# Kernel tuning notes

Hardware: AMD Instinct MI355X
Metric: run time of the kernel (lower is better)

## Reference

```python
import jax, jax.numpy as jnp
import numpy as np

IMG = 800.0
STRIDE = 16
P = 7            # pool_out_size
SAMP = 2         # RoIAlign samples per bin per dim (sampling_ratio=-1 approximated as 2)
SCALE = 1.0 / 16.0   # feature_compress
TOPN = 6000      # score_top_n
NMS_TOPN = 300   # nms_top_n
NMS_TH = 0.7
NC = 21


def _anchors(H, W):
    ratios = np.array([0.5, 1.0, 2.0])
    scales = np.array([8.0, 16.0, 32.0])
    ws = (STRIDE * scales[None, :] / np.sqrt(ratios)[:, None]).reshape(-1)  # [9]
    hs = (STRIDE * scales[None, :] * np.sqrt(ratios)[:, None]).reshape(-1)
    cx = (np.arange(W) + 0.5) * STRIDE
    cy = (np.arange(H) + 0.5) * STRIDE
    cxg, cyg = np.meshgrid(cx, cy)  # [H,W]
    a = np.stack([cxg[..., None] - ws / 2, cyg[..., None] - hs / 2,
                  cxg[..., None] + ws / 2, cyg[..., None] + hs / 2], axis=-1)  # [H,W,9,4]
    return jnp.asarray(a.reshape(-1, 4), jnp.float32)


def _decode(anchors, deltas):
    aw = anchors[:, 2] - anchors[:, 0]
    ah = anchors[:, 3] - anchors[:, 1]
    ax = anchors[:, 0] + aw / 2
    ay = anchors[:, 1] + ah / 2
    cx = ax + deltas[:, 0] * aw
    cy = ay + deltas[:, 1] * ah
    w = aw * jnp.exp(deltas[:, 2])
    h = ah * jnp.exp(deltas[:, 3])
    boxes = jnp.stack([cx - w / 2, cy - h / 2, cx + w / 2, cy + h / 2], axis=1)
    return jnp.clip(boxes, 0.0, IMG)


def _iou(b):
    area = (b[:, 2] - b[:, 0]) * (b[:, 3] - b[:, 1])
    lt = jnp.maximum(b[:, None, :2], b[None, :, :2])
    rb = jnp.minimum(b[:, None, 2:], b[None, :, 2:])
    wh = jnp.clip(rb - lt, 0.0)
    inter = wh[..., 0] * wh[..., 1]
    return inter / (area[:, None] + area[None, :] - inter + 1e-9)


def _nms_select(boxes, scores):
    # boxes already sorted descending by scores; greedy NMS, fixed-size output indices
    iou = _iou(boxes)
    n = boxes.shape[0]
    rng = jnp.arange(n)

    def body(i, sup):
        keep_i = jnp.logical_not(sup[i])
        return sup | (keep_i & (iou[i] > NMS_TH) & (rng > i))

    sup = jax.lax.fori_loop(0, n, body, jnp.zeros((n,), bool))
    sel = jnp.where(sup, -jnp.inf, scores)
    _, idx = jax.lax.top_k(sel, NMS_TOPN)
    return idx


def _roi_align(feat, rois):
    # feat [C,H,W], rois [R,4] in image coords
    C, H, W = feat.shape
    off = (jnp.arange(P * SAMP, dtype=jnp.float32) + 0.5) / SAMP  # bin-unit positions

    def one(box):
        x1, y1, x2, y2 = box * SCALE
        xs = x1 + off * (x2 - x1) / P  # [P*SAMP]
        ys = y1 + off * (y2 - y1) / P
        x0 = jnp.floor(xs)
        y0 = jnp.floor(ys)
        lx = xs - x0
        ly = ys - y0
        x0i = jnp.clip(x0, 0, W - 1).astype(jnp.int32)
        x1i = jnp.clip(x0 + 1, 0, W - 1).astype(jnp.int32)
        y0i = jnp.clip(y0, 0, H - 1).astype(jnp.int32)
        y1i = jnp.clip(y0 + 1, 0, H - 1).astype(jnp.int32)

        def g(yi, xi):
            return feat[:, yi[:, None], xi[None, :]]  # [C,PS,PS]

        v = (g(y0i, x0i) * ((1 - ly)[:, None] * (1 - lx)[None, :])[None]
             + g(y0i, x1i) * ((1 - ly)[:, None] * lx[None, :])[None]
             + g(y1i, x0i) * (ly[:, None] * (1 - lx)[None, :])[None]
             + g(y1i, x1i) * (ly[:, None] * lx[None, :])[None])
        return v.reshape(C, P, SAMP, P, SAMP).mean(axis=(2, 4))  # [C,P,P]

    return jax.vmap(one)(rois)  # [R,C,P,P]


def reference(image, w_feat, b_feat, w_rpn, b_rpn, w_score, b_score,
              w_delta, b_delta, w_fc7, b_fc7, w_cls, b_cls, w_reg, b_reg):
    # backbone: stride-16 patchifying conv -> [1,512,50,50]
    feat = jax.lax.conv_general_dilated(image, w_feat, (STRIDE, STRIDE), 'VALID') \
           + b_feat[None, :, None, None]
    H, W = feat.shape[2], feat.shape[3]
    anchors = _anchors(H, W)  # [H*W*9, 4]

    # RPN: 3x3 conv + relu, 1x1 score/delta heads
    h = jax.nn.relu(jax.lax.conv_general_dilated(feat, w_rpn, (1, 1), 'SAME')
                    + b_rpn[None, :, None, None])
    sc = jnp.einsum('bchw,oc->bhwo', h, w_score) + b_score  # [1,H,W,9*2]
    dl = jnp.einsum('bchw,oc->bhwo', h, w_delta) + b_delta  # [1,H,W,9*4]
    rpn_score = jax.nn.softmax(sc.reshape(-1, 2), axis=-1)  # [HW*9, 2]
    rpn_delta = dl.reshape(-1, 4)

    # compute_proposals: decode, clip, top-k by fg score, greedy NMS
    fg = rpn_score[:, 1]
    boxes = _decode(anchors, rpn_delta)
    top_s, top_i = jax.lax.top_k(jax.lax.stop_gradient(fg), TOPN)
    cand = boxes[top_i]
    keep = _nms_select(jax.lax.stop_gradient(cand), top_s)
    rois = cand[keep]  # [300,4]

    # RoIAlign + heads
    pool = _roi_align(feat[0], rois)  # [300,512,7,7]
    fc7 = jax.nn.relu(pool.reshape(pool.shape[0], -1) @ w_fc7.T + b_fc7)  # [300,4096]
    score = fc7 @ w_cls.T + b_cls  # [300,21]
    bbox = (fc7 @ w_reg.T + b_reg).reshape(-1, NC, 4)  # [300,21,4]
    return score, bbox


def setup_inputs():
    key = jax.random.key(0)
    ks = jax.random.split(key, 9)

    def rn(k, shape, s=0.02):
        return jax.random.normal(k, shape, jnp.float32) * s

    z = lambda n: jnp.zeros((n,), jnp.float32)
    return {
        'image': jax.random.normal(ks[0], (1, 3, 800, 800), jnp.float32),
        'w_feat': rn(ks[1], (512, 3, 16, 16)), 'b_feat': z(512),
        'w_rpn': rn(ks[2], (512, 512, 3, 3)), 'b_rpn': z(512),
        'w_score': rn(ks[3], (18, 512)), 'b_score': z(18),
        'w_delta': rn(ks[4], (36, 512), 0.01), 'b_delta': z(36),
        'w_fc7': rn(ks[5], (4096, 512 * 7 * 7), 0.01), 'b_fc7': z(4096),
        'w_cls': rn(ks[6], (21, 4096)), 'b_cls': z(21),
        'w_reg': rn(ks[7], (84, 4096)), 'b_reg': z(84),
    }
```

## Files before the change

kernel.cpp:

```cpp
#include <hip/hip_runtime.h>
#include <cstdint>

typedef short  short8  __attribute__((ext_vector_type(8)));
typedef unsigned short ushort8 __attribute__((ext_vector_type(8)));
typedef _Float16 half8 __attribute__((ext_vector_type(8)));
typedef float  f32x4   __attribute__((ext_vector_type(4)));
typedef unsigned long long u64;

#define NPOS 2500
#define NA   22500
#define TOPN 6000
#define NKEEP 300
#define NBUCK 65536
#define THRESH 512
#define NSUB 8192
#define KSTEPS 392
#define RANKBLKS 22

__device__ __forceinline__ unsigned short f2bf(float f) {
  unsigned u = __float_as_uint(f);
  return (unsigned short)((u + 0x7FFFu + ((u >> 16) & 1u)) >> 16);
}

__global__ __launch_bounds__(256) void k1_gemm(const float* __restrict__ Asrc,
    const float* __restrict__ Bsrc, float* __restrict__ P, int klen,
    const float* __restrict__ wr, unsigned short* __restrict__ Whi,
    unsigned short* __restrict__ Wlo, int* __restrict__ histbuf)
{
  {
    int gtid = ((blockIdx.z * gridDim.y + blockIdx.y) * gridDim.x + blockIdx.x) * 256
             + threadIdx.x;
    int nth = gridDim.x * gridDim.y * gridDim.z * 256;
    if (gtid < NBUCK + 1 + 256) histbuf[gtid] = 0;
    for (int e = gtid; e < 512 * 4608; e += nth) {
      int n = e / 4608, r = e - n * 4608;
      int s = r >> 9, c = r & 511;
      float w = wr[n * 4608 + c * 9 + s] * 1024.f;
      _Float16 hi = (_Float16)w;
      _Float16 lo = (_Float16)(w - (float)hi);
      ((_Float16*)Whi)[e] = hi;
      ((_Float16*)Wlo)[e] = lo;
    }
  }

  __shared__ float As[32][128];
  __shared__ float Bs[32][132];
  int tid = threadIdx.x;
  int tx = tid & 15, ty = tid >> 4;
  int mt = blockIdx.x, nt = blockIdx.y;
  int m0 = mt * 128, n0 = nt * 128;
  int kbase = blockIdx.z * klen;

  int m_loc = tid & 127;
  int half = tid >> 7;
  int gm = m0 + m_loc;
  int y = gm / 50, x = gm - y * 50;
  bool mok = gm < NPOS;

  float acc[8][8] = {};

  for (int kt = 0; kt < klen; kt += 32) {
    int kb = kbase + kt;
    int k0 = kb + half * 16;
    int ci = k0 >> 8, r = (k0 >> 4) & 15;
    const float* src = Asrc + ci * 640000 + (y * 16 + r) * 800 + x * 16;
#pragma unroll
    for (int j = 0; j < 4; ++j) {
      float4 v = mok ? *(const float4*)(src + j * 4) : make_float4(0.f, 0.f, 0.f, 0.f);
      As[half * 16 + j * 4 + 0][m_loc] = v.x;
      As[half * 16 + j * 4 + 1][m_loc] = v.y;
      As[half * 16 + j * 4 + 2][m_loc] = v.z;
      As[half * 16 + j * 4 + 3][m_loc] = v.w;
    }
#pragma unroll
    for (int i = 0; i < 4; ++i) {
      int e = i * 256 + tid;
      int k4 = e & 7, n = e >> 3;
      float4 v = *(const float4*)(Bsrc + (size_t)(n0 + n) * 768 + kb + k4 * 4);
      Bs[k4 * 4 + 0][n] = v.x;
      Bs[k4 * 4 + 1][n] = v.y;
      Bs[k4 * 4 + 2][n] = v.z;
      Bs[k4 * 4 + 3][n] = v.w;
    }
    __syncthreads();
#pragma unroll 8
    for (int k = 0; k < 32; ++k) {
      float4 a0 = *(const float4*)&As[k][ty * 8];
      float4 a1 = *(const float4*)&As[k][ty * 8 + 4];
      float4 b0 = *(const float4*)&Bs[k][tx * 8];
      float4 b1 = *(const float4*)&Bs[k][tx * 8 + 4];
      float av[8] = {a0.x, a0.y, a0.z, a0.w, a1.x, a1.y, a1.z, a1.w};
      float bv[8] = {b0.x, b0.y, b0.z, b0.w, b1.x, b1.y, b1.z, b1.w};
#pragma unroll
      for (int i2 = 0; i2 < 8; ++i2)
#pragma unroll
        for (int j2 = 0; j2 < 8; ++j2) acc[i2][j2] += av[i2] * bv[j2];
    }
    __syncthreads();
  }
  float* Pp = P + ((size_t)(blockIdx.z * 20 + mt) * 4 + nt) * 16384;
#pragma unroll
  for (int i = 0; i < 8; ++i) {
    float4 v0 = {acc[i][0], acc[i][1], acc[i][2], acc[i][3]};
    float4 v1 = {acc[i][4], acc[i][5], acc[i][6], acc[i][7]};
    *(float4*)&Pp[(ty * 8 + i) * 128 + tx * 8] = v0;
    *(float4*)&Pp[(ty * 8 + i) * 128 + tx * 8 + 4] = v1;
  }
}

__global__ __launch_bounds__(256) void kred1(const float* __restrict__ P,
    const float* __restrict__ bias, float* __restrict__ feat_t,
    unsigned short* __restrict__ Fhi, unsigned short* __restrict__ Flo, int KS)
{
  int idx = blockIdx.x * 256 + threadIdx.x;
  if (idx >= NPOS * 512) return;
  int m = idx >> 9, n = idx & 511;
  int mt = m >> 7, ml = m & 127, nt = n >> 7, nl = n & 127;
  float s = 0.f;
  for (int z = 0; z < KS; ++z)
    s += P[(((size_t)(z * 20 + mt) * 4 + nt) << 14) + ml * 128 + nl];
  s += bias[n];
  feat_t[idx] = s;
  float fs = s * 2048.f;
  _Float16 hi = (_Float16)fs;
  _Float16 lo = (_Float16)(fs - (float)hi);
  ((_Float16*)Fhi)[idx] = hi;
  ((_Float16*)Flo)[idx] = lo;
}

__global__ __launch_bounds__(256) void k2_mfma(
    const unsigned short* __restrict__ Fhi, const unsigned short* __restrict__ Flo,
    const unsigned short* __restrict__ Whi, const unsigned short* __restrict__ Wlo,
    float* __restrict__ partial)
{
  __shared__ __align__(16) unsigned short As[8 * 162 * 8];
  __shared__ __align__(16) unsigned short Bs[8 * 130 * 8];
  int tid = threadIdx.x;
  int lane = tid & 63, wn = tid >> 6;
  int nt = blockIdx.x, mt = blockIdx.y, z = blockIdx.z;
  int n0 = nt * 128;

  f32x4 acc[10][2];
#pragma unroll
  for (int i = 0; i < 10; ++i)
#pragma unroll
    for (int j = 0; j < 2; ++j) acc[i][j] = (f32x4){0.f, 0.f, 0.f, 0.f};

  int yv[5], xv[5], slotA[5], gof[5];
  bool okv[5];
#pragma unroll
  for (int j = 0; j < 5; ++j) {
    int o = j * 256 + tid;
    int m = o >> 3, g = o & 7;
    int gm = mt * 160 + m;
    okv[j] = gm < NPOS;
    yv[j] = gm / 50;
    xv[j] = gm - yv[j] * 50;
    slotA[j] = g * 162 + m;
    gof[j] = g * 8;
  }

  ushort8 aR[5], bR[4];

  auto LOAD = [&](int t) {
    int tg = z * 27 + t;
    const unsigned short* Asrc = (tg < 144) ? Fhi : Flo;
    const unsigned short* Bsrc = (tg < 72 || tg >= 144) ? Whi : Wlo;
    int ks = (tg >= 144) ? (tg - 144) : ((tg >= 72) ? (tg - 72) : tg);
    int ki = ks * 64;
    int srow = ki >> 9;
    int c0 = ki & 511;
    int dy = srow / 3, dx = srow - (srow / 3) * 3;
#pragma unroll
    for (int j = 0; j < 5; ++j) {
      int yy = yv[j] + dy - 1, xx = xv[j] + dx - 1;
      ushort8 v = {0, 0, 0, 0, 0, 0, 0, 0};
      if (okv[j] && (unsigned)yy < 50u && (unsigned)xx < 50u)
        v = *(const ushort8*)(Asrc + (size_t)(yy * 50 + xx) * 512 + c0 + gof[j]);
      aR[j] = v;
    }
#pragma unroll
    for (int j = 0; j < 4; ++j) {
      int o = j * 256 + tid;
      int n = o >> 3, g = o & 7;
      bR[j] = *(const ushort8*)(Bsrc + (size_t)(n0 + n) * 4608 + ki + g * 8);
    }
  };

  LOAD(0);
  for (int t = 0; t < 27; ++t) {
    __syncthreads();
#pragma unroll
    for (int j = 0; j < 5; ++j)
      ((ushort8*)As)[slotA[j]] = aR[j];
#pragma unroll
    for (int j = 0; j < 4; ++j) {
      int o = j * 256 + tid;
      ((ushort8*)Bs)[(o & 7) * 130 + (o >> 3)] = bR[j];
    }
    __syncthreads();
    if (t + 1 < 27) LOAD(t + 1);
#pragma unroll
    for (int kk = 0; kk < 2; ++kk) {
      int g = kk * 4 + (lane >> 4);
      half8 b0 = ((const half8*)Bs)[g * 130 + wn * 32 + (lane & 15)];
      half8 b1 = ((const half8*)Bs)[g * 130 + wn * 32 + 16 + (lane & 15)];
#pragma unroll
      for (int fm = 0; fm < 10; ++fm) {
        half8 a = ((const half8*)As)[g * 162 + fm * 16 + (lane & 15)];
        acc[fm][0] = __builtin_amdgcn_mfma_f32_16x16x32_f16(a, b0, acc[fm][0], 0, 0, 0);
        acc[fm][1] = __builtin_amdgcn_mfma_f32_16x16x32_f16(a, b1, acc[fm][1], 0, 0, 0);
      }
    }
  }
  float* P = partial + ((size_t)(z * 16 + mt) * 4 + nt) * 20480;
#pragma unroll
  for (int fm = 0; fm < 10; ++fm)
#pragma unroll
    for (int fn = 0; fn < 2; ++fn)
#pragma unroll
      for (int r = 0; r < 4; ++r) {
        int m = fm * 16 + (lane >> 4) * 4 + r;
        int n = wn * 32 + fn * 16 + (lane & 15);
        P[m * 128 + n] = acc[fm][fn][r];
      }
}

__global__ __launch_bounds__(256) void k3_fused(const float* __restrict__ P,
    const float* __restrict__ b_rpn,
    const float* __restrict__ w_score, const float* __restrict__ b_score,
    const float* __restrict__ w_delta, const float* __restrict__ b_delta,
    float4* __restrict__ boxes, u64* __restrict__ keys, int* __restrict__ hist)
{
  __shared__ float4 hv4[4][128];
  __shared__ float outv[4][54];
  int grp = threadIdx.x >> 6, lane = threadIdx.x & 63;
  int p = blockIdx.x * 4 + grp;
  int mt = p / 160, ml = p - mt * 160;
  int nt = lane >> 4;
  int nl8 = (lane * 8) & 127;

  float4 a0 = make_float4(0.f, 0.f, 0.f, 0.f);
  float4 a1 = make_float4(0.f, 0.f, 0.f, 0.f);
  for (int z = 0; z < 8; ++z) {
    const float* Pb = P + ((size_t)(z * 16 + mt) * 4 + nt) * 20480 + ml * 128 + nl8;
    float4 v0 = *(const float4*)Pb;
    float4 v1 = *(const float4*)(Pb + 4);
    a0.x += v0.x; a0.y += v0.y; a0.z += v0.z; a0.w += v0.w;
    a1.x += v1.x; a1.y += v1.y; a1.z += v1.z; a1.w += v1.w;
  }
  const float SC = 1.f / 2097152.f;
  const float4 b0 = *(const float4*)(b_rpn + lane * 8);
  const float4 b1 = *(const float4*)(b_rpn + lane * 8 + 4);
  float4 h0 = make_float4(fmaxf(a0.x * SC + b0.x, 0.f), fmaxf(a0.y * SC + b0.y, 0.f),
                          fmaxf(a0.z * SC + b0.z, 0.f), fmaxf(a0.w * SC + b0.w, 0.f));
  float4 h1 = make_float4(fmaxf(a1.x * SC + b1.x, 0.f), fmaxf(a1.y * SC + b1.y, 0.f),
                          fmaxf(a1.z * SC + b1.z, 0.f), fmaxf(a1.w * SC + b1.w, 0.f));
  hv4[grp][lane * 2] = h0;
  hv4[grp][lane * 2 + 1] = h1;
  __syncthreads();

  if (lane < 54) {
    const float* w; float bb;
    if (lane < 18) { w = w_score + lane * 512; bb = b_score[lane]; }
    else           { w = w_delta + (lane - 18) * 512; bb = b_delta[lane - 18]; }
    const float4* w4 = (const float4*)w;
    float s = 0.f;
#pragma unroll 4
    for (int q = 0; q < 128; ++q) {
      float4 a = hv4[grp][q], b = w4[q];
      s += a.x * b.x + a.y * b.y + a.z * b.z + a.w * b.w;
    }
    outv[grp][lane] = s + bb;
  }
  __syncthreads();
  if (lane < 9) {
    int k = lane;
    float s0 = outv[grp][2 * k], s1 = outv[grp][2 * k + 1];
    float mx = fmaxf(s0, s1);
    float e0 = expf(s0 - mx), e1 = expf(s1 - mx);
    float f = e1 / (e0 + e1);
    double ratio = (k < 3) ? 0.5 : ((k < 6) ? 1.0 : 2.0);
    int si = k - (k / 3) * 3;
    double scale = (si == 0) ? 8.0 : ((si == 1) ? 16.0 : 32.0);
    double sq = sqrt(ratio);
    double wsd = 16.0 * scale / sq;
    double hsd = 16.0 * scale * sq;
    int y = p / 50, x = p - (p / 50) * 50;
    double cxd = ((double)x + 0.5) * 16.0;
    double cyd = ((double)y + 0.5) * 16.0;
    float ax1 = (float)(cxd - wsd / 2.0);
    float ay1 = (float)(cyd - hsd / 2.0);
    float ax2 = (float)(cxd + wsd / 2.0);
    float ay2 = (float)(cyd + hsd / 2.0);
    float aw = ax2 - ax1, ah = ay2 - ay1;
    float axc = ax1 + aw * 0.5f, ayc = ay1 + ah * 0.5f;
    float d0 = outv[grp][18 + 4 * k], d1 = outv[grp][18 + 4 * k + 1];
    float d2 = outv[grp][18 + 4 * k + 2], d3 = outv[grp][18 + 4 * k + 3];
    float cx = axc + d0 * aw, cy = ayc + d1 * ah;
    float bw = aw * expf(d2), bh = ah * expf(d3);
    float bx1 = fminf(fmaxf(cx - bw * 0.5f, 0.f), 800.f);
    float by1 = fminf(fmaxf(cy - bh * 0.5f, 0.f), 800.f);
    float bx2 = fminf(fmaxf(cx + bw * 0.5f, 0.f), 800.f);
    float by2 = fminf(fmaxf(cy + bh * 0.5f, 0.f), 800.f);
    int idx = p * 9 + k;
    boxes[idx] = make_float4(bx1, by1, bx2, by2);
    u64 key = ((u64)__float_as_uint(f) << 32) | (u64)(0xFFFFFFFFu - (unsigned)idx);
    keys[idx] = key;
    atomicAdd(&hist[(unsigned)(key >> 46)], 1);
  }
}

__global__ __launch_bounds__(1024) void k4_scan(const int* __restrict__ hist,
    int* __restrict__ cur, int* __restrict__ nbig, int* __restrict__ wl)
{
  __shared__ int ps[1024];
  int t = threadIdx.x;
  int local[64];
  int s = 0;
#pragma unroll
  for (int j = 0; j < 64; ++j) { local[j] = hist[t * 64 + j]; s += local[j]; }
  int mysum = s;
  ps[t] = s;
  __syncthreads();
  for (int d = 1; d < 1024; d <<= 1) {
    int v = ps[t];
    int u = (t >= d) ? ps[t - d] : 0;
    __syncthreads();
    ps[t] = v + u;
    __syncthreads();
  }
  int base = ps[t] - mysum;
#pragma unroll
  for (int j = 0; j < 64; ++j) {
    int b = t * 64 + j;
    cur[b] = base;
    if (local[j] > THRESH) { int w = atomicAdd(nbig, 1); wl[w] = b; }
    base += local[j];
  }
}

__global__ __launch_bounds__(256) void k4_scatter(const u64* __restrict__ keys,
    int* __restrict__ cur, u64* __restrict__ membuf)
{
  int i = blockIdx.x * 256 + threadIdx.x;
  int lane = threadIdx.x & 63;
  bool valid = i < NA;
  u64 k = valid ? keys[i] : 0ull;
  unsigned b = (unsigned)(k >> 46);
  int pos = 0;
  u64 mask = __ballot(valid);
  while (mask) {
    int lead = __builtin_ctzll(mask);
    unsigned lb = (unsigned)__shfl((int)b, lead);
    u64 same = __ballot(valid && b == lb) & mask;
    int cnt = __popcll(same);
    int base = 0;
    if (lane == lead) base = atomicAdd(&cur[lb], cnt);
    base = __shfl(base, lead);
    if (valid && ((same >> lane) & 1ull)) {
      int rank = __popcll(same & ((1ull << lane) - 1ull));
      pos = base + rank;
    }
    mask &= ~same;
  }
  if (valid) membuf[pos] = k;
}

__global__ __launch_bounds__(1024) void k4_select(const u64* __restrict__ keys,
    const int* __restrict__ hist, const int* __restrict__ cur,
    const int* __restrict__ nbig, const int* __restrict__ wl,
    const u64* __restrict__ membuf, u64* __restrict__ membuf2,
    const float4* __restrict__ boxes, float4* __restrict__ cand,
    float* __restrict__ areas)
{
  __shared__ int cnt[NSUB];
  __shared__ int cur2[NSUB];
  __shared__ int ps[1024];
  int t = threadIdx.x;
  if (blockIdx.x < RANKBLKS) {
    int i = blockIdx.x * 1024 + t;
    if (i >= NA) return;
    u64 my = keys[i];
    unsigned b = (unsigned)(my >> 46);
    int cb = hist[b];
    if (cb > THRESH) return;
    int hi = cur[b];
    int lo = hi - cb;
    int r = NA - hi;
    for (int p = lo; p < hi; ++p) r += (membuf[p] > my) ? 1 : 0;
    if (r < TOPN) {
      unsigned idx = 0xFFFFFFFFu - (unsigned)my;
      float4 bx = boxes[idx];
      cand[r] = bx;
      areas[r] = (bx.z - bx.x) * (bx.w - bx.y);
    }
    return;
  }
  int nb = *nbig;
  for (int wi = blockIdx.x - RANKBLKS; wi < nb; wi += gridDim.x - RANKBLKS) {
    int b = wl[wi];
    int hi = cur[b], S = hist[b], lo = hi - S;
    for (int j = t; j < NSUB; j += 1024) cnt[j] = 0;
    __syncthreads();
    for (int e = lo + t; e < hi; e += 1024)
      atomicAdd(&cnt[(unsigned)(membuf[e] >> 33) & (NSUB - 1)], 1);
    __syncthreads();
    int loc[8], s = 0;
#pragma unroll
    for (int j = 0; j < 8; ++j) { loc[j] = cnt[t * 8 + j]; s += loc[j]; }
    ps[t] = s;
    __syncthreads();
    for (int d = 1; d < 1024; d <<= 1) {
      int v = ps[t];
      int u = (t >= d) ? ps[t - d] : 0;
      __syncthreads();
      ps[t] = v + u;
      __syncthreads();
    }
    int run = ps[1023] - ps[t];
#pragma unroll
    for (int j = 7; j >= 0; --j) {
      cur2[t * 8 + j] = lo + run;
      run += loc[j];
    }
    __syncthreads();
    for (int e = lo + t; e < hi; e += 1024) {
      u64 k = membuf[e];
      int p = atomicAdd(&cur2[(unsigned)(k >> 33) & (NSUB - 1)], 1);
      membuf2[p] = k;
    }
    __syncthreads();
    for (int e = lo + t; e < hi; e += 1024) {
      u64 my = membuf2[e];
      unsigned b2 = (unsigned)(my >> 33) & (NSUB - 1);
      int end = cur2[b2], start = end - cnt[b2];
      int r = (NA - hi) + (start - lo);
      for (int p = start; p < end; ++p) r += (membuf2[p] > my) ? 1 : 0;
      if (r < TOPN) {
        unsigned idx = 0xFFFFFFFFu - (unsigned)my;
        float4 bx = boxes[idx];
        cand[r] = bx;
        areas[r] = (bx.z - bx.x) * (bx.w - bx.y);
      }
    }
    __syncthreads();
  }
}

__global__ __launch_bounds__(256) void k5_iou(const float4* __restrict__ cand,
    const float* __restrict__ areas, u64* __restrict__ rowbuf)
{
  __shared__ float4 bj[64];
  __shared__ float aj[64];
  int jw = blockIdx.x;
  int i = blockIdx.y * 256 + threadIdx.x;
  if (threadIdx.x < 64) {
    int j = jw * 64 + threadIdx.x;
    bj[threadIdx.x] = (j < TOPN) ? cand[j] : make_float4(0.f, 0.f, 0.f, 0.f);
    aj[threadIdx.x] = (j < TOPN) ? areas[j] : 0.f;
  }
  __syncthreads();
  if (i >= TOPN) return;
  u64 word = 0ull;
  if (jw * 64 + 63 > i) {
    float4 bi = cand[i];
    float ai = areas[i];
#pragma unroll 8
    for (int b = 0; b < 64; ++b) {
      float4 bb = bj[b];
      float lx = fmaxf(bi.x, bb.x), ly = fmaxf(bi.y, bb.y);
      float rx = fminf(bi.z, bb.z), ry = fminf(bi.w, bb.w);
      float ww = fmaxf(rx - lx, 0.f), hh = fmaxf(ry - ly, 0.f);
      float inter = ww * hh;
      float iou = inter / (ai + aj[b] - inter + 1e-9f);
      int j = jw * 64 + b;
      if (iou > 0.7f && j > i && j < TOPN) word |= 1ull << b;
    }
  }
  rowbuf[(size_t)i * 96 + jw] = word;
}

__global__ __launch_bounds__(256) void k6_scan(const u64* __restrict__ rowbuf,
    const float4* __restrict__ cand, float4* __restrict__ rois)
{
  __shared__ u64 stage[64 * 97];
  __shared__ u64 sup[94];
  __shared__ int prefS[94];
  __shared__ int baseU_sh;
  int tid = threadIdx.x;
  if (tid < 94) sup[tid] = 0ull;
  if (tid == 0) baseU_sh = 0;

  u64 pre[24];
#pragma unroll
  for (int j = 0; j < 24; ++j) {
    int o = j * 256 + tid;
    int b = o / 94, w = o - b * 94;
    pre[j] = (o < 6016) ? rowbuf[(size_t)b * 96 + w] : 0ull;
  }
  __syncthreads();

  for (int c = 0; c < 94; ++c) {
#pragma unroll
    for (int j = 0; j < 24; ++j) {
      int o = j * 256 + tid;
      int b = o / 94, w = o - b * 94;
      if (o < 6016) stage[b * 97 + w] = pre[j];
    }
    __syncthreads();
    if (c + 1 < 94) {
#pragma unroll
      for (int j = 0; j < 24; ++j) {
        int o = j * 256 + tid;
        int b = o / 94, w = o - b * 94;
        pre[j] = (o < 6016) ? rowbuf[((size_t)(c + 1) * 64 + b) * 96 + w] : 0ull;
      }
    }
    u64 valid = (c == 93) ? ((1ull << 48) - 1ull) : ~0ull;
    u64 sup_c = sup[c];
    u64 live0 = ~sup_c & valid;
    u64 rw = stage[(tid & 63) * 97 + c];
    u64 live = live0, keep = 0ull;
    while (live) {
      int b = __builtin_ctzll(live);
      keep |= 1ull << b;
      u64 rb = (u64)__shfl((long long)rw, b);
      live &= ~rb;
      live &= ~(1ull << b);
    }
    int baseU = baseU_sh;
    if (tid < 64 && ((keep >> tid) & 1ull)) {
      u64 below = (tid == 0) ? 0ull : (keep & ((1ull << tid) - 1ull));
      int pos = baseU + __popcll(below);
      if (pos < NKEEP) rois[pos] = cand[c * 64 + tid];
    }
    __syncthreads();
    if (tid == 0) baseU_sh = baseU + __popcll(keep);
    if (tid == 64) sup[c] = sup_c | (live0 & ~keep);
    for (int w = c + 1 + tid; w < 94; w += 256) {
      u64 a = sup[w];
      u64 kk = keep;
      while (kk) {
        int b = __builtin_ctzll(kk);
        kk &= kk - 1;
        a |= stage[b * 97 + w];
      }
      sup[w] = a;
    }
    __syncthreads();
    if (baseU_sh >= NKEEP) break;
  }

  int totU = baseU_sh;
  if (totU < NKEEP) {
    if (tid == 0) {
      int s = 0;
      for (int w = 0; w < 94; ++w) { prefS[w] = s; s += __popcll(sup[w]); }
    }
    __syncthreads();
    for (int i = tid; i < TOPN; i += 256) {
      int w = i >> 6, b = i & 63;
      u64 sw = sup[w];
      if ((sw >> b) & 1ull) {
        u64 below = (b == 0) ? 0ull : (sw & ((1ull << b) - 1ull));
        int pos = totU + prefS[w] + __popcll(below);
        if (pos < NKEEP) rois[pos] = cand[i];
      }
    }
  }
}

__global__ __launch_bounds__(256) void k7_roi(const float4* __restrict__ rois,
    const float* __restrict__ feat_t, unsigned short* __restrict__ pool_bf)
{
  int r = blockIdx.x;
  int py = blockIdx.y / 7, px = blockIdx.y - (blockIdx.y / 7) * 7;
  int c = threadIdx.x;
  bool rok = r < NKEEP;
  float4 box = rok ? rois[r] : make_float4(0.f, 0.f, 0.f, 0.f);
  float x1 = box.x * 0.0625f, y1 = box.y * 0.0625f;
  float x2 = box.z * 0.0625f, y2 = box.w * 0.0625f;
  float acc0 = 0.f, acc1 = 0.f;
#pragma unroll
  for (int sy = 0; sy < 2; ++sy) {
#pragma unroll
    for (int sx = 0; sx < 2; ++sx) {
      float offx = ((float)(2 * px + sx) + 0.5f) * 0.5f;
      float offy = ((float)(2 * py + sy) + 0.5f) * 0.5f;
      float xs = x1 + (offx * (x2 - x1)) / 7.f;
      float ys = y1 + (offy * (y2 - y1)) / 7.f;
      float x0f = floorf(xs), y0f = floorf(ys);
      float lx = xs - x0f, ly = ys - y0f;
      int x0i = (int)fminf(fmaxf(x0f, 0.f), 49.f);
      int x1i = (int)fminf(fmaxf(x0f + 1.f, 0.f), 49.f);
      int y0i = (int)fminf(fmaxf(y0f, 0.f), 49.f);
      int y1i = (int)fminf(fmaxf(y0f + 1.f, 0.f), 49.f);
      const float* f00 = feat_t + (size_t)(y0i * 50 + x0i) * 512;
      const float* f01 = feat_t + (size_t)(y0i * 50 + x1i) * 512;
      const float* f10 = feat_t + (size_t)(y1i * 50 + x0i) * 512;
      const float* f11 = feat_t + (size_t)(y1i * 50 + x1i) * 512;
      float w00 = (1.f - ly) * (1.f - lx), w01 = (1.f - ly) * lx;
      float w10 = ly * (1.f - lx),          w11 = ly * lx;
      acc0 += w00 * f00[c] + w01 * f01[c] + w10 * f10[c] + w11 * f11[c];
      acc1 += w00 * f00[c + 256] + w01 * f01[c + 256] + w10 * f10[c + 256] + w11 * f11[c + 256];
    }
  }
  int k0 = c * 49 + py * 7 + px;
  int k1v = (c + 256) * 49 + py * 7 + px;
  unsigned short v0 = rok ? f2bf(acc0 * 0.25f) : (unsigned short)0;
  unsigned short v1 = rok ? f2bf(acc1 * 0.25f) : (unsigned short)0;
  pool_bf[(k0 >> 6) * 20480 + (((k0 >> 3) & 7) * 320 + r) * 8 + (k0 & 7)] = v0;
  pool_bf[(k1v >> 6) * 20480 + (((k1v >> 3) & 7) * 320 + r) * 8 + (k1v & 7)] = v1;
}

__global__ __launch_bounds__(512) void k8_gemm(const unsigned short* __restrict__ Ap,
    const float* __restrict__ W, float* __restrict__ partial, int spk)
{
  __shared__ __align__(16) unsigned short As[8 * 320 * 8];
  __shared__ __align__(16) unsigned short Bs[8 * 128 * 8];
  int tid = threadIdx.x;
  int lane = tid & 63, wv = tid >> 6;
  int wm = wv & 1, wn = wv >> 1;
  int n0 = blockIdx.x * 128;
  int by = blockIdx.y;
  int steps = min(spk, KSTEPS - by * spk);

  f32x4 acc[10][2];
#pragma unroll
  for (int i = 0; i < 10; ++i)
#pragma unroll
    for (int j = 0; j < 2; ++j) acc[i][j] = (f32x4){0.f, 0.f, 0.f, 0.f};

  ushort8 aReg[5];
  float4 wReg[4];

  auto LOAD = [&](int t) {
    size_t abase = (size_t)(by * spk + t) * 20480;
    int k0 = (by * spk + t) * 64;
#pragma unroll
    for (int j = 0; j < 5; ++j)
      aReg[j] = *(const ushort8*)(Ap + abase + (size_t)(j * 512 + tid) * 8);
#pragma unroll
    for (int j = 0; j < 4; ++j) {
      int fq = j * 512 + tid;
      int n = fq >> 4, kq = fq & 15;
      wReg[j] = *(const float4*)(W + (size_t)(n0 + n) * 25088 + k0 + kq * 4);
    }
  };

  LOAD(0);
  for (int t = 0; t < steps; ++t) {
    u64 pk[4];
#pragma unroll
    for (int j = 0; j < 4; ++j) {
      float4 v = wReg[j];
      pk[j] = (u64)f2bf(v.x) | ((u64)f2bf(v.y) << 16)
            | ((u64)f2bf(v.z) << 32) | ((u64)f2bf(v.w) << 48);
    }
    __syncthreads();
#pragma unroll
    for (int j = 0; j < 5; ++j)
      ((ushort8*)As)[j * 512 + tid] = aReg[j];
#pragma unroll
    for (int j = 0; j < 4; ++j) {
      int fq = j * 512 + tid;
      int n = fq >> 4, kq = fq & 15;
      *(u64*)&Bs[((kq >> 1) * 128 + n) * 8 + (kq & 1) * 4] = pk[j];
    }
    __syncthreads();
    if (t + 1 < steps) LOAD(t + 1);
#pragma unroll
    for (int kk = 0; kk < 2; ++kk) {
      int g = kk * 4 + (lane >> 4);
      short8 b0 = ((const short8*)Bs)[g * 128 + wn * 32 + (lane & 15)];
      short8 b1 = ((const short8*)Bs)[g * 128 + wn * 32 + 16 + (lane & 15)];
#pragma unroll
      for (int fm = 0; fm < 10; ++fm) {
        short8 a = ((const short8*)As)[g * 320 + wm * 160 + fm * 16 + (lane & 15)];
        acc[fm][0] = __builtin_amdgcn_mfma_f32_16x16x32_bf16(a, b0, acc[fm][0], 0, 0, 0);
        acc[fm][1] = __builtin_amdgcn_mfma_f32_16x16x32_bf16(a, b1, acc[fm][1], 0, 0, 0);
      }
    }
  }
  float* P = partial + (size_t)(by * 32 + blockIdx.x) * (320 * 128);
#pragma unroll
  for (int fm = 0; fm < 10; ++fm)
#pragma unroll
    for (int fn = 0; fn < 2; ++fn)
#pragma unroll
      for (int r = 0; r < 4; ++r) {
        int m = wm * 160 + fm * 16 + (lane >> 4) * 4 + r;
        int n = wn * 32 + fn * 16 + (lane & 15);
        P[m * 128 + n] = acc[fm][fn][r];
      }
}

__global__ __launch_bounds__(256) void k9a_reduce(const float* __restrict__ partial,
    const float* __restrict__ bias, float* __restrict__ fc7, int KS)
{
  int idx = blockIdx.x * 256 + threadIdx.x;
  if (idx >= 300 * 4096) return;
  int m = idx >> 12, n = idx & 4095;
  int nt = n >> 7, nn = n & 127;
  float s = 0.f;
  for (int ks = 0; ks < KS; ++ks)
    s += partial[((size_t)(ks * 32 + nt) * 320 + m) * 128 + nn];
  s += bias[n];
  fc7[idx] = fmaxf(s, 0.f);
}

__global__ __launch_bounds__(256) void k9b_heads(const float* __restrict__ fc7,
    const float* __restrict__ wc, const float* __restrict__ bc,
    const float* __restrict__ wr, const float* __restrict__ br,
    float* __restrict__ out)
{
  int wid = blockIdx.x * 4 + (threadIdx.x >> 6);
  int lane = threadIdx.x & 63;
  if (wid >= 300 * 105) return;
  int m = wid / 105, o = wid - m * 105;
  const float* w; float b;
  if (o < 21) { w = wc + (size_t)o * 4096; b = bc[o]; }
  else        { w = wr + (size_t)(o - 21) * 4096; b = br[o - 21]; }
  const float4* f4 = (const float4*)(fc7 + (size_t)m * 4096);
  const float4* w4 = (const float4*)w;
  float s = 0.f;
#pragma unroll
  for (int i = 0; i < 16; ++i) {
    float4 a = f4[i * 64 + lane];
    float4 ww = w4[i * 64 + lane];
    s += a.x * ww.x + a.y * ww.y + a.z * ww.z + a.w * ww.w;
  }
#pragma unroll
  for (int d = 32; d > 0; d >>= 1) s += __shfl_down(s, d);
  if (lane == 0) {
    s += b;
    if (o < 21) out[m * 21 + o] = s;
    else        out[6300 + m * 84 + (o - 21)] = s;
  }
}

extern "C" void kernel_launch(void* const* d_in, const int* in_sizes, int n_in,
                              void* d_out, int out_size, void* d_ws, size_t ws_size,
                              hipStream_t stream)
{
  (void)in_sizes; (void)n_in; (void)out_size;
  const float* img    = (const float*)d_in[0];
  const float* w_feat = (const float*)d_in[1];
  const float* b_feat = (const float*)d_in[2];
  const float* w_rpn  = (const float*)d_in[3];
  const float* b_rpn  = (const float*)d_in[4];
  const float* w_score= (const float*)d_in[5];
  const float* b_score= (const float*)d_in[6];
  const float* w_delta= (const float*)d_in[7];
  const float* b_delta= (const float*)d_in[8];
  const float* w_fc7  = (const float*)d_in[9];
  const float* b_fc7  = (const float*)d_in[10];
  const float* w_cls  = (const float*)d_in[11];
  const float* b_cls  = (const float*)d_in[12];
  const float* w_reg  = (const float*)d_in[13];
  const float* b_reg  = (const float*)d_in[14];
  float* out = (float*)d_out;

  char* ws = (char*)d_ws;
  size_t off = 0;
  auto alloc = [&](size_t bytes) -> void* {
    void* p = ws + off;
    off = (off + bytes + 511) & ~(size_t)511;
    return p;
  };
  float* feat_t  = (float*)alloc(5120000);
  unsigned short* Fhi = (unsigned short*)alloc((size_t)NPOS * 512 * 2);
  unsigned short* Flo = (unsigned short*)alloc((size_t)NPOS * 512 * 2);
  unsigned short* Whi = (unsigned short*)alloc((size_t)512 * 4608 * 2);
  unsigned short* Wlo = (unsigned short*)alloc((size_t)512 * 4608 * 2);
  float4* boxes  = (float4*)alloc((size_t)NA * 16);
  u64* keys      = (u64*)alloc((size_t)NA * 8);
  int* histbuf   = (int*)alloc((size_t)(NBUCK + 1 + 256) * 4);
  int* hist = histbuf; int* nbig = histbuf + NBUCK; int* wl = histbuf + NBUCK + 1;
  int* bcur      = (int*)alloc((size_t)NBUCK * 4);
  u64* membuf    = (u64*)alloc((size_t)NA * 8);
  u64* membuf2   = (u64*)alloc((size_t)NA * 8);
  float4* cand   = (float4*)alloc((size_t)TOPN * 16);
  float* areas   = (float*)alloc((size_t)TOPN * 4);
  u64* rowbuf    = (u64*)alloc((size_t)TOPN * 96 * 8);
  float4* rois   = (float4*)alloc(NKEEP * 16);
  unsigned short* pool_bf = (unsigned short*)alloc((size_t)KSTEPS * 20480 * 2);
  float* fc7     = (float*)alloc((size_t)300 * 4096 * 4);

  size_t avail = (ws_size > off) ? (ws_size - off) : 0;
  float* P_sh = (float*)(ws + off);
  int KS1 = 8, KS8 = 8;
  while (KS1 > 1 && (size_t)KS1 * 80 * 16384 * 4 > avail) KS1 >>= 1;
  while (KS8 > 1 && (size_t)KS8 * 32 * 320 * 128 * 4 > avail) KS8 >>= 1;
  int klen1 = 768 / KS1;
  int spk8 = (KSTEPS + KS8 - 1) / KS8;

  k1_gemm<<<dim3(20, 4, KS1), 256, 0, stream>>>(img, w_feat, P_sh, klen1,
                                                w_rpn, Whi, Wlo, histbuf);
  kred1<<<(NPOS * 512 + 255) / 256, 256, 0, stream>>>(P_sh, b_feat, feat_t, Fhi, Flo, KS1);
  k2_mfma<<<dim3(4, 16, 8), 256, 0, stream>>>(Fhi, Flo, Whi, Wlo, P_sh);
  k3_fused<<<625, 256, 0, stream>>>(P_sh, b_rpn, w_score, b_score, w_delta, b_delta,
                                    boxes, keys, hist);
  k4_scan   <<<1, 1024, 0, stream>>>(hist, bcur, nbig, wl);
  k4_scatter<<<88, 256, 0, stream>>>(keys, bcur, membuf);
  k4_select <<<RANKBLKS + 64, 1024, 0, stream>>>(keys, hist, bcur, nbig, wl,
                                                 membuf, membuf2, boxes, cand, areas);
  k5_iou    <<<dim3(94, 24), 256, 0, stream>>>(cand, areas, rowbuf);
  k6_scan   <<<1, 256, 0, stream>>>(rowbuf, cand, rois);
  k7_roi    <<<dim3(320, 49), 256, 0, stream>>>(rois, feat_t, pool_bf);
  k8_gemm   <<<dim3(32, KS8), 512, 0, stream>>>(pool_bf, w_fc7, P_sh, spk8);
  k9a_reduce<<<(300 * 4096 + 255) / 256, 256, 0, stream>>>(P_sh, b_fc7, fc7, KS8);
  k9b_heads<<<(300 * 105 + 3) / 4, 256, 0, stream>>>(fc7, w_cls, b_cls, w_reg, b_reg, out);
}
```

Baseline: 609.7 us.

## Split weight prep into own kernel and remap RoIAlign threads to output tiles

The RPN weight split into fp16 hi/lo halves and the histogram zeroing move out of the first GEMM into a separate kernel. That kernel stages each weight row in shared memory so the transposed reads are coalesced. RoIAlign now assigns one thread per RoI and eight consecutive K indices, so each thread writes one 16-byte vector in the packed bf16 layout instead of scattering 2-byte stores. The cost is that feature reads become gathers where adjacent threads (different RoIs) touch unrelated addresses, and the bilinear coordinate math is recomputed for every element.

Measured after the change: 844.1 us. 38.4% more time.

```diff
diff --git a/kernel.cpp b/kernel.cpp
--- a/kernel.cpp
+++ b/kernel.cpp
@@ -22,27 +22,31 @@
   return (unsigned short)((u + 0x7FFFu + ((u >> 16) & 1u)) >> 16);
 }
 
+__global__ __launch_bounds__(256) void kw_prep(const float* __restrict__ wr,
+    unsigned short* __restrict__ Whi, unsigned short* __restrict__ Wlo,
+    int* __restrict__ histbuf)
+{
+  __shared__ float wrow[4608];
+  int n = blockIdx.x, tid = threadIdx.x;
+  {
+    int gtid = n * 256 + tid;
+    if (gtid < NBUCK + 1 + 256) histbuf[gtid] = 0;
+  }
+  for (int i = tid; i < 4608; i += 256) wrow[i] = wr[(size_t)n * 4608 + i];
+  __syncthreads();
+  for (int o = tid; o < 4608; o += 256) {
+    int s = o >> 9, c = o & 511;
+    float w = wrow[c * 9 + s] * 1024.f;
+    _Float16 hi = (_Float16)w;
+    _Float16 lo = (_Float16)(w - (float)hi);
+    ((_Float16*)Whi)[(size_t)n * 4608 + o] = hi;
+    ((_Float16*)Wlo)[(size_t)n * 4608 + o] = lo;
+  }
+}
+
 __global__ __launch_bounds__(256) void k1_gemm(const float* __restrict__ Asrc,
-    const float* __restrict__ Bsrc, float* __restrict__ P, int klen,
-    const float* __restrict__ wr, unsigned short* __restrict__ Whi,
-    unsigned short* __restrict__ Wlo, int* __restrict__ histbuf)
-{
-  {
-    int gtid = ((blockIdx.z * gridDim.y + blockIdx.y) * gridDim.x + blockIdx.x) * 256
-             + threadIdx.x;
-    int nth = gridDim.x * gridDim.y * gridDim.z * 256;
-    if (gtid < NBUCK + 1 + 256) histbuf[gtid] = 0;
-    for (int e = gtid; e < 512 * 4608; e += nth) {
-      int n = e / 4608, r = e - n * 4608;
-      int s = r >> 9, c = r & 511;
-      float w = wr[n * 4608 + c * 9 + s] * 1024.f;
-      _Float16 hi = (_Float16)w;
-      _Float16 lo = (_Float16)(w - (float)hi);
-      ((_Float16*)Whi)[e] = hi;
-      ((_Float16*)Wlo)[e] = lo;
-    }
-  }
-
+    const float* __restrict__ Bsrc, float* __restrict__ P, int klen)
+{
   __shared__ float As[32][128];
   __shared__ float Bs[32][132];
   int tid = threadIdx.x;
@@ -571,47 +575,51 @@
   }
 }
 
-__global__ __launch_bounds__(256) void k7_roi(const float4* __restrict__ rois,
+__global__ __launch_bounds__(320) void k7_roi(const float4* __restrict__ rois,
     const float* __restrict__ feat_t, unsigned short* __restrict__ pool_bf)
 {
-  int r = blockIdx.x;
-  int py = blockIdx.y / 7, px = blockIdx.y - (blockIdx.y / 7) * 7;
-  int c = threadIdx.x;
-  bool rok = r < NKEEP;
-  float4 box = rok ? rois[r] : make_float4(0.f, 0.f, 0.f, 0.f);
+  int step = blockIdx.x >> 3, g = blockIdx.x & 7;
+  int m = threadIdx.x;
+  bool rok = m < NKEEP;
+  float4 box = rok ? rois[m] : make_float4(0.f, 0.f, 0.f, 0.f);
   float x1 = box.x * 0.0625f, y1 = box.y * 0.0625f;
   float x2 = box.z * 0.0625f, y2 = box.w * 0.0625f;
-  float acc0 = 0.f, acc1 = 0.f;
-#pragma unroll
-  for (int sy = 0; sy < 2; ++sy) {
-#pragma unroll
-    for (int sx = 0; sx < 2; ++sx) {
-      float offx = ((float)(2 * px + sx) + 0.5f) * 0.5f;
-      float offy = ((float)(2 * py + sy) + 0.5f) * 0.5f;
-      float xs = x1 + (offx * (x2 - x1)) / 7.f;
-      float ys = y1 + (offy * (y2 - y1)) / 7.f;
-      float x0f = floorf(xs), y0f = floorf(ys);
-      float lx = xs - x0f, ly = ys - y0f;
-      int x0i = (int)fminf(fmaxf(x0f, 0.f), 49.f);
-      int x1i = (int)fminf(fmaxf(x0f + 1.f, 0.f), 49.f);
-      int y0i = (int)fminf(fmaxf(y0f, 0.f), 49.f);
-      int y1i = (int)fminf(fmaxf(y0f + 1.f, 0.f), 49.f);
-      const float* f00 = feat_t + (size_t)(y0i * 50 + x0i) * 512;
-      const float* f01 = feat_t + (size_t)(y0i * 50 + x1i) * 512;
-      const float* f10 = feat_t + (size_t)(y1i * 50 + x0i) * 512;
-      const float* f11 = feat_t + (size_t)(y1i * 50 + x1i) * 512;
-      float w00 = (1.f - ly) * (1.f - lx), w01 = (1.f - ly) * lx;
-      float w10 = ly * (1.f - lx),          w11 = ly * lx;
-      acc0 += w00 * f00[c] + w01 * f01[c] + w10 * f10[c] + w11 * f11[c];
-      acc1 += w00 * f00[c + 256] + w01 * f01[c + 256] + w10 * f10[c + 256] + w11 * f11[c + 256];
-    }
-  }
-  int k0 = c * 49 + py * 7 + px;
-  int k1v = (c + 256) * 49 + py * 7 + px;
-  unsigned short v0 = rok ? f2bf(acc0 * 0.25f) : (unsigned short)0;
-  unsigned short v1 = rok ? f2bf(acc1 * 0.25f) : (unsigned short)0;
-  pool_bf[(k0 >> 6) * 20480 + (((k0 >> 3) & 7) * 320 + r) * 8 + (k0 & 7)] = v0;
-  pool_bf[(k1v >> 6) * 20480 + (((k1v >> 3) & 7) * 320 + r) * 8 + (k1v & 7)] = v1;
+  float dxs = (x2 - x1) / 7.f, dys = (y2 - y1) / 7.f;
+  int kbase = step * 64 + g * 8;
+
+  ushort8 outv;
+#pragma unroll
+  for (int e = 0; e < 8; ++e) {
+    int k = kbase + e;
+    int c = k / 49;
+    int s = k - c * 49;
+    int py = s / 7, px = s - (s / 7) * 7;
+    float acc = 0.f;
+#pragma unroll
+    for (int sy = 0; sy < 2; ++sy) {
+#pragma unroll
+      for (int sx = 0; sx < 2; ++sx) {
+        float offx = ((float)(2 * px + sx) + 0.5f) * 0.5f;
+        float offy = ((float)(2 * py + sy) + 0.5f) * 0.5f;
+        float xs = x1 + offx * dxs;
+        float ys = y1 + offy * dys;
+        float x0f = floorf(xs), y0f = floorf(ys);
+        float lx = xs - x0f, ly = ys - y0f;
+        int x0i = (int)fminf(fmaxf(x0f, 0.f), 49.f);
+        int x1i = (int)fminf(fmaxf(x0f + 1.f, 0.f), 49.f);
+        int y0i = (int)fminf(fmaxf(y0f, 0.f), 49.f);
+        int y1i = (int)fminf(fmaxf(y0f + 1.f, 0.f), 49.f);
+        float f00 = feat_t[(size_t)(y0i * 50 + x0i) * 512 + c];
+        float f01 = feat_t[(size_t)(y0i * 50 + x1i) * 512 + c];
+        float f10 = feat_t[(size_t)(y1i * 50 + x0i) * 512 + c];
+        float f11 = feat_t[(size_t)(y1i * 50 + x1i) * 512 + c];
+        acc += (1.f - ly) * (1.f - lx) * f00 + (1.f - ly) * lx * f01
+             + ly * (1.f - lx) * f10 + ly * lx * f11;
+      }
+    }
+    outv[e] = rok ? f2bf(acc * 0.25f) : (unsigned short)0;
+  }
+  *(ushort8*)&pool_bf[(size_t)step * 20480 + (g * 320 + m) * 8] = outv;
 }
 
 __global__ __launch_bounds__(512) void k8_gemm(const unsigned short* __restrict__ Ap,
@@ -796,8 +804,8 @@
   int klen1 = 768 / KS1;
   int spk8 = (KSTEPS + KS8 - 1) / KS8;
 
-  k1_gemm<<<dim3(20, 4, KS1), 256, 0, stream>>>(img, w_feat, P_sh, klen1,
-                                                w_rpn, Whi, Wlo, histbuf);
+  kw_prep<<<512, 256, 0, stream>>>(w_rpn, Whi, Wlo, histbuf);
+  k1_gemm<<<dim3(20, 4, KS1), 256, 0, stream>>>(img, w_feat, P_sh, klen1);
   kred1<<<(NPOS * 512 + 255) / 256, 256, 0, stream>>>(P_sh, b_feat, feat_t, Fhi, Flo, KS1);
   k2_mfma<<<dim3(4, 16, 8), 256, 0, stream>>>(Fhi, Flo, Whi, Wlo, P_sh);
   k3_fused<<<625, 256, 0, stream>>>(P_sh, b_rpn, w_score, b_score, w_delta, b_delta,
@@ -808,7 +816,7 @@
                                                  membuf, membuf2, boxes, cand, areas);
   k5_iou    <<<dim3(94, 24), 256, 0, stream>>>(cand, areas, rowbuf);
   k6_scan   <<<1, 256, 0, stream>>>(rowbuf, cand, rois);
-  k7_roi    <<<dim3(320, 49), 256, 0, stream>>>(rois, feat_t, pool_bf);
+  k7_roi    <<<3136, 320, 0, stream>>>(rois, feat_t, pool_bf);
   k8_gemm   <<<dim3(32, KS8), 512, 0, stream>>>(pool_bf, w_fc7, P_sh, spk8);
   k9a_reduce<<<(300 * 4096 + 255) / 256, 256, 0, stream>>>(P_sh, b_fc7, fc7, KS8);
   k9b_heads<<<(300 * 105 + 3) / 4, 256, 0, stream>>>(fc7, w_cls, b_cls, w_reg, b_reg, out);
```
